# Performance work log

Measured on AMD Instinct MI355X. Metric: run time of the kernel, lower is better.

Reference implementation:

```python
import jax, jax.numpy as jnp
import numpy as np

D = 256; DFFN = 1024; H = 8; NLVL = 4; NPNT = 4; HD = D // H
BS = 4; NQ = 100; NPTS = 25
SPATIAL = [(128, 128), (64, 64), (32, 32), (16, 16)]
LEN_IN = sum(h * w for h, w in SPATIAL)


def _ln(x, g, b, eps=1e-5):
    m = x.mean(-1, keepdims=True)
    v = ((x - m) ** 2).mean(-1, keepdims=True)
    return (x - m) * jax.lax.rsqrt(v + eps) * g + b


def _mha(q, k, v, w_in, b_in, w_out, b_out):
    # torch nn.MultiheadAttention math, batch-first layout [B,S,D]
    B, Sq, _ = q.shape; Sk = k.shape[1]
    wq, wk, wv = jnp.split(w_in, 3, 0); bq, bk, bv = jnp.split(b_in, 3)
    qh = (q @ wq.T + bq).reshape(B, Sq, H, HD).transpose(0, 2, 1, 3)
    kh = (k @ wk.T + bk).reshape(B, Sk, H, HD).transpose(0, 2, 1, 3)
    vh = (v @ wv.T + bv).reshape(B, Sk, H, HD).transpose(0, 2, 1, 3)
    a = jax.nn.softmax(jnp.einsum('bhqd,bhkd->bhqk', qh, kh) * (1.0 / float(np.sqrt(HD))), -1)
    o = jnp.einsum('bhqk,bhkd->bhqd', a, vh).transpose(0, 2, 1, 3).reshape(B, Sq, D)
    return o @ w_out.T + b_out


def _msdeform(query, ref, src, off_w, off_b, aw_w, aw_b, val_w, val_b, out_w, out_b):
    # MSDeformAttn: per-query multi-level bilinear sampling + weighted aggregation
    bs, Lq, _ = query.shape
    value = (src @ val_w.T + val_b).reshape(bs, LEN_IN, H, HD)
    off = (query @ off_w.T + off_b).reshape(bs, Lq, H, NLVL, NPNT, 2)
    aw = jax.nn.softmax((query @ aw_w.T + aw_b).reshape(bs, Lq, H, NLVL * NPNT), -1)
    aw = aw.reshape(bs, Lq, H, NLVL, NPNT)
    norm = jnp.array([[w, h] for h, w in SPATIAL], jnp.float32)  # (W,H) per level
    loc = ref[:, :, None, :, None, :] + off / norm[None, None, None, :, None, :]
    out = jnp.zeros((bs, H, Lq, HD), query.dtype)
    start = 0
    for l, (hh, ww) in enumerate(SPATIAL):
        v_l = value[:, start:start + hh * ww].transpose(0, 2, 1, 3)  # [bs,H,hw,HD]
        start += hh * ww
        # grid_sample align_corners=False pixel coords: loc*size - 0.5
        x = (loc[:, :, :, l, :, 0] * ww - 0.5).transpose(0, 2, 1, 3).reshape(bs, H, Lq * NPNT)
        y = (loc[:, :, :, l, :, 1] * hh - 0.5).transpose(0, 2, 1, 3).reshape(bs, H, Lq * NPNT)
        x0 = jnp.floor(x); y0 = jnp.floor(y); wx = x - x0; wy = y - y0
        x0i = x0.astype(jnp.int32); y0i = y0.astype(jnp.int32); x1i = x0i + 1; y1i = y0i + 1
        def g(xi, yi):
            valid = ((xi >= 0) & (xi < ww) & (yi >= 0) & (yi < hh)).astype(query.dtype)
            idx = jnp.clip(yi, 0, hh - 1) * ww + jnp.clip(xi, 0, ww - 1)
            return jnp.take_along_axis(v_l, idx[..., None], axis=2) * valid[..., None]
        s = (g(x0i, y0i) * ((1 - wx) * (1 - wy))[..., None]
             + g(x1i, y0i) * (wx * (1 - wy))[..., None]
             + g(x0i, y1i) * ((1 - wx) * wy)[..., None]
             + g(x1i, y1i) * (wx * wy)[..., None])
        s = s.reshape(bs, H, Lq, NPNT, HD)
        out = out + (s * aw[:, :, :, l].transpose(0, 2, 1, 3)[..., None]).sum(3)
    return out.transpose(0, 2, 1, 3).reshape(bs, Lq, D) @ out_w.T + out_b


def _fwd(tgt, query_pos, reference_points, src,
         w_in_intra, b_in_intra, w_out_intra, b_out_intra, g_norm_intra, b_norm_intra,
         w_in_inter, b_in_inter, w_out_inter, b_out_inter, g_norm_inter, b_norm_inter,
         off_w, off_b, aw_w, aw_b, val_w, val_b, co_w, co_b, g_norm_cross, b_norm_cross,
         lin1_w, lin1_b, lin2_w, lin2_b, g_norm3, b_norm3):
    bs, nq, npts, d = tgt.shape
    # intra-instance self-attention (over control points)
    q = (tgt + query_pos).reshape(bs * nq, npts, d)
    t2 = _mha(q, q, tgt.reshape(bs * nq, npts, d), w_in_intra, b_in_intra, w_out_intra, b_out_intra)
    tgt = _ln(tgt + t2.reshape(bs, nq, npts, d), g_norm_intra, b_norm_intra)
    # inter-instance self-attention (over queries), no pos embed per source code
    ti = tgt.transpose(0, 2, 1, 3).reshape(bs * npts, nq, d)
    t2 = _mha(ti, ti, ti, w_in_inter, b_in_inter, w_out_inter, b_out_inter)
    ti = _ln(ti + t2, g_norm_inter, b_norm_inter).reshape(bs, npts, nq, d).transpose(0, 2, 1, 3)
    # deformable cross-attention
    ref = jnp.broadcast_to(reference_points[:, :, None], (bs, nq, npts, NLVL, 2)).reshape(bs, nq * npts, NLVL, 2)
    qc = (ti + query_pos).reshape(bs, nq * npts, d)
    t2 = _msdeform(qc, ref, src, off_w, off_b, aw_w, aw_b, val_w, val_b, co_w, co_b).reshape(bs, nq, npts, d)
    tgt = _ln(ti + t2, g_norm_cross, b_norm_cross)
    # FFN
    ff = jax.nn.relu(tgt @ lin1_w.T + lin1_b) @ lin2_w.T + lin2_b
    return _ln(tgt + ff, g_norm3, b_norm3)


def setup_inputs() -> dict:
    key = jax.random.key(0)
    ki = iter(jax.random.split(key, 40))
    def rn(shape, sc=0.02):
        return jax.random.normal(next(ki), shape, jnp.float32) * sc
    inp = dict(
        tgt=jax.random.normal(next(ki), (BS, NQ, NPTS, D), jnp.float32),
        query_pos=jax.random.normal(next(ki), (BS, NQ, NPTS, D), jnp.float32),
        reference_points=jax.random.uniform(next(ki), (BS, NQ, NLVL, 2), jnp.float32),
        src=jax.random.normal(next(ki), (BS, LEN_IN, D), jnp.float32),
        w_in_intra=rn((3 * D, D)), b_in_intra=jnp.zeros((3 * D,), jnp.float32),
        w_out_intra=rn((D, D)), b_out_intra=jnp.zeros((D,), jnp.float32),
        g_norm_intra=jnp.ones((D,), jnp.float32), b_norm_intra=jnp.zeros((D,), jnp.float32),
        w_in_inter=rn((3 * D, D)), b_in_inter=jnp.zeros((3 * D,), jnp.float32),
        w_out_inter=rn((D, D)), b_out_inter=jnp.zeros((D,), jnp.float32),
        g_norm_inter=jnp.ones((D,), jnp.float32), b_norm_inter=jnp.zeros((D,), jnp.float32),
        off_w=rn((H * NLVL * NPNT * 2, D), 0.001), off_b=rn((H * NLVL * NPNT * 2,), 0.5),
        aw_w=rn((H * NLVL * NPNT, D)), aw_b=jnp.zeros((H * NLVL * NPNT,), jnp.float32),
        val_w=rn((D, D)), val_b=jnp.zeros((D,), jnp.float32),
        co_w=rn((D, D)), co_b=jnp.zeros((D,), jnp.float32),
        g_norm_cross=jnp.ones((D,), jnp.float32), b_norm_cross=jnp.zeros((D,), jnp.float32),
        lin1_w=rn((DFFN, D)), lin1_b=jnp.zeros((DFFN,), jnp.float32),
        lin2_w=rn((D, DFFN)), lin2_b=jnp.zeros((D,), jnp.float32),
        g_norm3=jnp.ones((D,), jnp.float32), b_norm3=jnp.zeros((D,), jnp.float32),
        src_spatial_shapes=jnp.array(SPATIAL, jnp.int32),
        level_start_index=jnp.array(np.cumsum([0] + [h * w for h, w in SPATIAL[:-1]]), jnp.int32),
    )
    return inp


def reference(tgt, query_pos, reference_points, src,
              w_in_intra, b_in_intra, w_out_intra, b_out_intra, g_norm_intra, b_norm_intra,
              w_in_inter, b_in_inter, w_out_inter, b_out_inter, g_norm_inter, b_norm_inter,
              off_w, off_b, aw_w, aw_b, val_w, val_b, co_w, co_b, g_norm_cross, b_norm_cross,
              lin1_w, lin1_b, lin2_w, lin2_b, g_norm3, b_norm3,
              src_spatial_shapes, level_start_index):
    # spatial shapes / level starts are compile-time constants (SPATIAL); args kept for signature parity
    return _fwd(tgt, query_pos, reference_points, src,
                w_in_intra, b_in_intra, w_out_intra, b_out_intra, g_norm_intra, b_norm_intra,
                w_in_inter, b_in_inter, w_out_inter, b_out_inter, g_norm_inter, b_norm_inter,
                off_w, off_b, aw_w, aw_b, val_w, val_b, co_w, co_b, g_norm_cross, b_norm_cross,
                lin1_w, lin1_b, lin2_w, lin2_b, g_norm3, b_norm3)
```

## Files before the change

### kernel.cpp

```cpp
#include <hip/hip_runtime.h>
#include <math.h>

#define DMODEL 256
#define HEADS  8
#define HDIM   32
#define BS     4
#define NQ     100
#define NPTS   25
#define LQ     2500
#define M10K   10000
#define LEN_IN 21760
#define MVAL   87040

typedef float f32x4 __attribute__((ext_vector_type(4)));
typedef short s16x8 __attribute__((ext_vector_type(8)));
typedef unsigned short u16;

static __device__ __forceinline__ short f2bf(float f) {
    unsigned u = __builtin_bit_cast(unsigned, f);
    u = (u + 0x7fffu + ((u >> 16) & 1u)) >> 16;
    return (short)u;
}
static __device__ __forceinline__ unsigned pack2(float lo, float hi) {
    return (unsigned)(u16)f2bf(lo) | ((unsigned)(u16)f2bf(hi) << 16);
}
static __device__ __forceinline__ float bf_lo(unsigned u) {
    return __builtin_bit_cast(float, u << 16);
}
static __device__ __forceinline__ float bf_hi(unsigned u) {
    return __builtin_bit_cast(float, u & 0xffff0000u);
}

__global__ __launch_bounds__(256) void convert_weights_kernel(
    const float* __restrict__ s0, const float* __restrict__ s1,
    const float* __restrict__ s2, const float* __restrict__ s3,
    const float* __restrict__ s4, const float* __restrict__ s5,
    const float* __restrict__ s6, const float* __restrict__ s7,
    const float* __restrict__ s8, const float* __restrict__ s9,
    u16* __restrict__ dst)
{
    int t8 = (blockIdx.x * 256 + threadIdx.x) * 8;
    if (t8 >= 1277952) return;
    const float* s; int base;
    if      (t8 <  196608) { s = s0; base = 0;       }
    else if (t8 <  262144) { s = s1; base = 196608;  }
    else if (t8 <  458752) { s = s2; base = 262144;  }
    else if (t8 <  524288) { s = s3; base = 458752;  }
    else if (t8 <  589824) { s = s4; base = 524288;  }
    else if (t8 <  622592) { s = s5; base = 589824;  }
    else if (t8 <  688128) { s = s6; base = 622592;  }
    else if (t8 <  753664) { s = s7; base = 688128;  }
    else if (t8 < 1015808) { s = s8; base = 753664;  }
    else                   { s = s9; base = 1015808; }
    const float* p = s + (t8 - base);
    float4 a = *(const float4*)p;
    float4 b = *(const float4*)(p + 4);
    s16x8 v;
    v[0]=f2bf(a.x); v[1]=f2bf(a.y); v[2]=f2bf(a.z); v[3]=f2bf(a.w);
    v[4]=f2bf(b.x); v[5]=f2bf(b.y); v[6]=f2bf(b.z); v[7]=f2bf(b.w);
    *(s16x8*)(dst + t8) = v;
}

__global__ __launch_bounds__(256) void add_convert_kernel(
    const float* __restrict__ a, const float* __restrict__ b,
    u16* __restrict__ xb, u16* __restrict__ ab, int n8)
{
    int i = blockIdx.x * 256 + threadIdx.x;
    if (i >= n8) return;
    size_t o = (size_t)i * 8;
    float4 a0 = *(const float4*)(a + o);
    float4 a1 = *(const float4*)(a + o + 4);
    if (ab) {
        s16x8 v;
        v[0]=f2bf(a0.x); v[1]=f2bf(a0.y); v[2]=f2bf(a0.z); v[3]=f2bf(a0.w);
        v[4]=f2bf(a1.x); v[5]=f2bf(a1.y); v[6]=f2bf(a1.z); v[7]=f2bf(a1.w);
        *(s16x8*)(ab + o) = v;
    }
    if (b) {
        float4 b0 = *(const float4*)(b + o);
        float4 b1 = *(const float4*)(b + o + 4);
        a0.x += b0.x; a0.y += b0.y; a0.z += b0.z; a0.w += b0.w;
        a1.x += b1.x; a1.y += b1.y; a1.z += b1.z; a1.w += b1.w;
    }
    s16x8 v;
    v[0]=f2bf(a0.x); v[1]=f2bf(a0.y); v[2]=f2bf(a0.z); v[3]=f2bf(a0.w);
    v[4]=f2bf(a1.x); v[5]=f2bf(a1.y); v[6]=f2bf(a1.z); v[7]=f2bf(a1.w);
    *(s16x8*)(xb + o) = v;
}

#define LDSK 40

__global__ __launch_bounds__(256) void gemm_mfma_kernel(
    const void* __restrict__ Av, int a_bf16, int lda,
    const u16* __restrict__ W, int K,
    const float* __restrict__ bias,
    void* __restrict__ Cv, int ldc,
    int M, int relu, int out_bf16)
{
    __shared__ short As[64 * LDSK];
    __shared__ short Ws[64 * LDSK];

    const int tid = threadIdx.x;
    const int m0 = blockIdx.y * 64, n0 = blockIdx.x * 64;

    const int srow = tid >> 2;
    const int skseg = (tid & 3) * 8;

    const int wave = tid >> 6;
    const int wm = wave & 1, wn = wave >> 1;
    const int lane = tid & 63;
    const int lrow = lane & 15;
    const int kq = lane >> 4;

    f32x4 acc[2][2];
#pragma unroll
    for (int i = 0; i < 2; ++i)
#pragma unroll
        for (int j = 0; j < 2; ++j) acc[i][j] = (f32x4)(0.f);

    for (int k0 = 0; k0 < K; k0 += 32) {
        int gm = m0 + srow;
        s16x8 av = (s16x8)0;
        if (a_bf16) {
            if (gm < M)
                av = *(const s16x8*)((const u16*)Av + (size_t)gm * lda + k0 + skseg);
        } else {
            if (gm < M) {
                const float* ap = (const float*)Av + (size_t)gm * lda + k0 + skseg;
                float4 a0 = *(const float4*)ap;
                float4 a1 = *(const float4*)(ap + 4);
                av[0]=f2bf(a0.x); av[1]=f2bf(a0.y); av[2]=f2bf(a0.z); av[3]=f2bf(a0.w);
                av[4]=f2bf(a1.x); av[5]=f2bf(a1.y); av[6]=f2bf(a1.z); av[7]=f2bf(a1.w);
            }
        }
        s16x8 wv = *(const s16x8*)(W + (size_t)(n0 + srow) * K + k0 + skseg);
        *(s16x8*)&As[srow * LDSK + skseg] = av;
        *(s16x8*)&Ws[srow * LDSK + skseg] = wv;
        __syncthreads();

        s16x8 af[2], bf[2];
#pragma unroll
        for (int i = 0; i < 2; ++i)
            af[i] = *(const s16x8*)&As[(wm * 32 + i * 16 + lrow) * LDSK + kq * 8];
#pragma unroll
        for (int j = 0; j < 2; ++j)
            bf[j] = *(const s16x8*)&Ws[(wn * 32 + j * 16 + lrow) * LDSK + kq * 8];
#pragma unroll
        for (int i = 0; i < 2; ++i)
#pragma unroll
            for (int j = 0; j < 2; ++j)
                acc[i][j] = __builtin_amdgcn_mfma_f32_16x16x32_bf16(af[i], bf[j], acc[i][j], 0, 0, 0);
        __syncthreads();
    }

#pragma unroll
    for (int i = 0; i < 2; ++i) {
#pragma unroll
        for (int j = 0; j < 2; ++j) {
            int col = n0 + wn * 32 + j * 16 + lrow;
            float bv = bias[col];
#pragma unroll
            for (int reg = 0; reg < 4; ++reg) {
                int gm = m0 + wm * 32 + i * 16 + kq * 4 + reg;
                if (gm < M) {
                    float v = acc[i][j][reg] + bv;
                    if (relu) v = fmaxf(v, 0.f);
                    if (out_bf16)
                        ((u16*)Cv)[(size_t)gm * ldc + col] = (u16)f2bf(v);
                    else
                        ((float*)Cv)[(size_t)gm * ldc + col] = v;
                }
            }
        }
    }
}

__global__ void small_attn_kernel(const float* __restrict__ qkv,
                                  u16* __restrict__ out,
                                  int S, float scale)
{
    extern __shared__ float lds[];
    const int b = blockIdx.x, h = blockIdx.y;
    const float* base = qkv + (size_t)b * S * 768;

    for (int idx = threadIdx.x; idx < S * 64; idx += blockDim.x) {
        int r = idx >> 6, c = idx & 63;
        float v = (c < 32) ? base[r * 768 + 256 + h * 32 + c]
                           : base[r * 768 + 512 + h * 32 + (c - 32)];
        lds[idx] = v;
    }
    __syncthreads();

    const int i = threadIdx.x;
    if (i < S) {
        float q[32];
        const float* qp = base + i * 768 + h * 32;
#pragma unroll
        for (int c = 0; c < 32; ++c) q[c] = qp[c];
        float m = -1e30f, l = 0.f, acc[32];
#pragma unroll
        for (int c = 0; c < 32; ++c) acc[c] = 0.f;
        for (int j = 0; j < S; ++j) {
            const float* kj = &lds[j * 64];
            float s = 0.f;
#pragma unroll
            for (int c = 0; c < 32; ++c) s = fmaf(q[c], kj[c], s);
            s *= scale;
            float mn = fmaxf(m, s);
            float alpha = __expf(m - mn);
            float p = __expf(s - mn);
            l = l * alpha + p;
            const float* vj = kj + 32;
#pragma unroll
            for (int c = 0; c < 32; ++c) acc[c] = acc[c] * alpha + p * vj[c];
            m = mn;
        }
        float inv = 1.f / l;
        unsigned* op = (unsigned*)(out + ((size_t)b * S + i) * 256 + h * 32);
#pragma unroll
        for (int c = 0; c < 16; ++c)
            op[c] = pack2(acc[2 * c] * inv, acc[2 * c + 1] * inv);
    }
}

__global__ __launch_bounds__(64) void add_ln_kernel(
    const float* __restrict__ a, const float* __restrict__ b,
    const float* __restrict__ g, const float* __restrict__ beta,
    float* __restrict__ out, u16* __restrict__ out_bf, int transpose_mode)
{
    const int r = blockIdx.x;
    const int lane = threadIdx.x;
    const float* ar = a + (size_t)r * 256;
    const float* br = b + (size_t)r * 256;
    float x[4];
    float s = 0.f;
#pragma unroll
    for (int i = 0; i < 4; ++i) {
        x[i] = ar[lane + 64 * i] + br[lane + 64 * i];
        s += x[i];
    }
#pragma unroll
    for (int off = 32; off >= 1; off >>= 1) s += __shfl_xor(s, off);
    float mean = s * (1.f / 256.f);
    float vs = 0.f;
#pragma unroll
    for (int i = 0; i < 4; ++i) { float d = x[i] - mean; vs += d * d; }
#pragma unroll
    for (int off = 32; off >= 1; off >>= 1) vs += __shfl_xor(vs, off);
    float rstd = rsqrtf(vs * (1.f / 256.f) + 1e-5f);

    size_t ro = r;
    if (transpose_mode) {
        int q = r % 100; int bp = r / 100; int p = bp % 25; int bb = bp / 25;
        ro = ((size_t)bb * 100 + q) * 25 + p;
    }
    float* orow = out + ro * 256;
    u16* brow = out_bf ? out_bf + ro * 256 : (u16*)0;
#pragma unroll
    for (int i = 0; i < 4; ++i) {
        int c = lane + 64 * i;
        float v = (x[i] - mean) * rstd * g[c] + beta[c];
        orow[c] = v;
        if (brow) brow[c] = (u16)f2bf(v);
    }
}

__global__ __launch_bounds__(64) void tgt_to_ti_kernel(
    const float* __restrict__ tgt1, float* __restrict__ ti, u16* __restrict__ tib)
{
    const int r = blockIdx.x;
    int q = r % 100; int bp = r / 100; int p = bp % 25; int b = bp / 25;
    const float4* srcp = (const float4*)(tgt1 + (((size_t)b * 100 + q) * 25 + p) * 256);
    float4 v = srcp[threadIdx.x];
    ((float4*)(ti + (size_t)r * 256))[threadIdx.x] = v;
    uint2 pk = make_uint2(pack2(v.x, v.y), pack2(v.z, v.w));
    ((uint2*)(tib + (size_t)r * 256))[threadIdx.x] = pk;
}

__global__ __launch_bounds__(256, 4) void msdeform_sample_kernel(
    const u16* __restrict__ value,
    const float* __restrict__ off,
    const float* __restrict__ awl,
    const float* __restrict__ refp,
    u16* __restrict__ sampled)
{
    const int unit = blockIdx.x * 8 + (threadIdx.x >> 5);
    const int t = threadIdx.x & 31;
    const int h = t >> 2, c8 = t & 3;
    const int b = unit / LQ, lq = unit - b * LQ;
    const int q = lq / NPTS;

    const float* awp = awl + (size_t)unit * 128 + h * 16;
    float w[16];
    float mx = -1e30f;
#pragma unroll
    for (int k = 0; k < 16; ++k) { w[k] = awp[k]; mx = fmaxf(mx, w[k]); }
    float sum = 0.f;
#pragma unroll
    for (int k = 0; k < 16; ++k) { w[k] = __expf(w[k] - mx); sum += w[k]; }
    const float inv = 1.f / sum;

    const float* offp = off + (size_t)unit * 256 + h * 32;
    const float* rp = refp + ((size_t)b * 100 + q) * 8;
    const u16* vbase = value + (size_t)b * LEN_IN * 256 + h * 32 + c8 * 8;

    float acc[8];
#pragma unroll
    for (int k = 0; k < 8; ++k) acc[k] = 0.f;

    int start = 0;
    const int sz[4] = {128, 64, 32, 16};
#pragma unroll
    for (int l = 0; l < 4; ++l) {
        const int hh = sz[l], ww = sz[l];
        const float rx = rp[l * 2 + 0], ry = rp[l * 2 + 1];
#pragma unroll 1
        for (int pt = 0; pt < 4; ++pt) {
            float ox = offp[(l * 4 + pt) * 2 + 0];
            float oy = offp[(l * 4 + pt) * 2 + 1];
            float x = rx * ww + ox - 0.5f;
            float y = ry * hh + oy - 0.5f;
            float x0f = floorf(x), y0f = floorf(y);
            float wx = x - x0f, wy = y - y0f;
            int x0 = (int)x0f, y0 = (int)y0f;
            int x1 = x0 + 1, y1 = y0 + 1;
            float aw = w[l * 4 + pt] * inv;

            int x0c = min(max(x0, 0), ww - 1), x1c = min(max(x1, 0), ww - 1);
            int y0c = min(max(y0, 0), hh - 1), y1c = min(max(y1, 0), hh - 1);
            float w00 = aw * (1.f - wx) * (1.f - wy);
            float w10 = aw * wx * (1.f - wy);
            float w01 = aw * (1.f - wx) * wy;
            float w11 = aw * wx * wy;
            if (!(x0 >= 0 && x0 < ww)) { w00 = 0.f; w01 = 0.f; }
            if (!(x1 >= 0 && x1 < ww)) { w10 = 0.f; w11 = 0.f; }
            if (!(y0 >= 0 && y0 < hh)) { w00 = 0.f; w10 = 0.f; }
            if (!(y1 >= 0 && y1 < hh)) { w01 = 0.f; w11 = 0.f; }

            uint4 u00 = *(const uint4*)(vbase + (size_t)(start + y0c * ww + x0c) * 256);
            uint4 u10 = *(const uint4*)(vbase + (size_t)(start + y0c * ww + x1c) * 256);
            uint4 u01 = *(const uint4*)(vbase + (size_t)(start + y1c * ww + x0c) * 256);
            uint4 u11 = *(const uint4*)(vbase + (size_t)(start + y1c * ww + x1c) * 256);

#define ACC4(u, wgt) \
            acc[0] = fmaf(wgt, bf_lo(u.x), acc[0]); \
            acc[1] = fmaf(wgt, bf_hi(u.x), acc[1]); \
            acc[2] = fmaf(wgt, bf_lo(u.y), acc[2]); \
            acc[3] = fmaf(wgt, bf_hi(u.y), acc[3]); \
            acc[4] = fmaf(wgt, bf_lo(u.z), acc[4]); \
            acc[5] = fmaf(wgt, bf_hi(u.z), acc[5]); \
            acc[6] = fmaf(wgt, bf_lo(u.w), acc[6]); \
            acc[7] = fmaf(wgt, bf_hi(u.w), acc[7]);
            ACC4(u00, w00); ACC4(u10, w10); ACC4(u01, w01); ACC4(u11, w11);
#undef ACC4
        }
        start += hh * ww;
    }

    uint4 pk;
    pk.x = pack2(acc[0], acc[1]); pk.y = pack2(acc[2], acc[3]);
    pk.z = pack2(acc[4], acc[5]); pk.w = pack2(acc[6], acc[7]);
    *(uint4*)(sampled + (size_t)unit * 256 + h * 32 + c8 * 8) = pk;
}

extern "C" void kernel_launch(void* const* d_in, const int* in_sizes, int n_in,
                              void* d_out, int out_size, void* d_ws, size_t ws_size,
                              hipStream_t stream)
{
    (void)in_sizes; (void)n_in; (void)out_size; (void)ws_size;

    const float* tgt        = (const float*)d_in[0];
    const float* query_pos  = (const float*)d_in[1];
    const float* refp       = (const float*)d_in[2];
    const float* src        = (const float*)d_in[3];
    const float* w_in_intra = (const float*)d_in[4];
    const float* b_in_intra = (const float*)d_in[5];
    const float* w_out_intra= (const float*)d_in[6];
    const float* b_out_intra= (const float*)d_in[7];
    const float* g_ln_intra = (const float*)d_in[8];
    const float* b_ln_intra = (const float*)d_in[9];
    const float* w_in_inter = (const float*)d_in[10];
    const float* b_in_inter = (const float*)d_in[11];
    const float* w_out_inter= (const float*)d_in[12];
    const float* b_out_inter= (const float*)d_in[13];
    const float* g_ln_inter = (const float*)d_in[14];
    const float* b_ln_inter = (const float*)d_in[15];
    const float* off_w      = (const float*)d_in[16];
    const float* off_b      = (const float*)d_in[17];
    const float* aw_w       = (const float*)d_in[18];
    const float* aw_b       = (const float*)d_in[19];
    const float* val_w      = (const float*)d_in[20];
    const float* val_b      = (const float*)d_in[21];
    const float* co_w       = (const float*)d_in[22];
    const float* co_b       = (const float*)d_in[23];
    const float* g_ln_cross = (const float*)d_in[24];
    const float* b_ln_cross = (const float*)d_in[25];
    const float* lin1_w     = (const float*)d_in[26];
    const float* lin1_b     = (const float*)d_in[27];
    const float* lin2_w     = (const float*)d_in[28];
    const float* lin2_b     = (const float*)d_in[29];
    const float* g_ln3      = (const float*)d_in[30];
    const float* b_ln3      = (const float*)d_in[31];

    float* ws    = (float*)d_ws;
    float* qkv   = ws;
    float* tmp   = ws + 7680000;
    u16*   attnb = (u16*)(ws + 10240000);
    float* tgt1  = ws + 11520000;
    float* ti    = ws + 14080000;
    u16*   tib   = (u16*)(ws + 16640000);
    float* tA    = ws + 17920000;
    u16*   qcb   = (u16*)(ws + 20480000);
    u16*   x1b   = (u16*)(ws + 21760000);
    u16*   tgtb  = (u16*)(ws + 23040000);
    float* awl   = ws + 24320000;
    u16*   valueb= (u16*)(ws + 25600000);
    u16*   wb    = (u16*)(ws + 36741120);
    float* out   = (float*)d_out;

    u16* wb_in_intra  = wb;
    u16* wb_out_intra = wb + 196608;
    u16* wb_in_inter  = wb + 262144;
    u16* wb_out_inter = wb + 458752;
    u16* wb_off       = wb + 524288;
    u16* wb_aw        = wb + 589824;
    u16* wb_val       = wb + 622592;
    u16* wb_co        = wb + 688128;
    u16* wb_lin1      = wb + 753664;
    u16* wb_lin2      = wb + 1015808;

    const float scale = 0.17677669529663687f;
    const int MB10K = (M10K + 63) / 64;

    convert_weights_kernel<<<624, 256, 0, stream>>>(
        w_in_intra, w_out_intra, w_in_inter, w_out_inter, off_w,
        aw_w, val_w, co_w, lin1_w, lin2_w, wb);
    add_convert_kernel<<<1250, 256, 0, stream>>>(tgt, query_pos, x1b, tgtb, 320000);

    gemm_mfma_kernel<<<dim3(8, MB10K), 256, 0, stream>>>(x1b, 1, 256, wb_in_intra, 256,
                                                         b_in_intra, qkv, 768, M10K, 0, 0);
    gemm_mfma_kernel<<<dim3(4, MB10K), 256, 0, stream>>>(tgtb, 1, 256, wb_in_intra + 512 * 256, 256,
                                                         b_in_intra + 512, qkv + 512, 768, M10K, 0, 0);
    small_attn_kernel<<<dim3(400, 8), 64, 25 * 64 * 4, stream>>>(qkv, attnb, 25, scale);
    gemm_mfma_kernel<<<dim3(4, MB10K), 256, 0, stream>>>(attnb, 1, 256, wb_out_intra, 256,
                                                         b_out_intra, tmp, 256, M10K, 0, 0);
    add_ln_kernel<<<M10K, 64, 0, stream>>>(tgt, tmp, g_ln_intra, b_ln_intra, tgt1, (u16*)0, 0);

    tgt_to_ti_kernel<<<M10K, 64, 0, stream>>>(tgt1, ti, tib);
    gemm_mfma_kernel<<<dim3(12, MB10K), 256, 0, stream>>>(tib, 1, 256, wb_in_inter, 256,
                                                          b_in_inter, qkv, 768, M10K, 0, 0);
    small_attn_kernel<<<dim3(100, 8), 128, 100 * 64 * 4, stream>>>(qkv, attnb, 100, scale);
    gemm_mfma_kernel<<<dim3(4, MB10K), 256, 0, stream>>>(attnb, 1, 256, wb_out_inter, 256,
                                                         b_out_inter, tmp, 256, M10K, 0, 0);
    add_ln_kernel<<<M10K, 64, 0, stream>>>(ti, tmp, g_ln_inter, b_ln_inter, tA, (u16*)0, 1);

    add_convert_kernel<<<1250, 256, 0, stream>>>(tA, query_pos, qcb, (u16*)0, 320000);
    gemm_mfma_kernel<<<dim3(4, 1360), 256, 0, stream>>>(src, 0, 256, wb_val, 256,
                                                        val_b, valueb, 256, MVAL, 0, 1);
    gemm_mfma_kernel<<<dim3(4, MB10K), 256, 0, stream>>>(qcb, 1, 256, wb_off, 256,
                                                         off_b, tgt1, 256, M10K, 0, 0);
    gemm_mfma_kernel<<<dim3(2, MB10K), 256, 0, stream>>>(qcb, 1, 256, wb_aw, 256,
                                                         aw_b, awl, 128, M10K, 0, 0);
    msdeform_sample_kernel<<<1250, 256, 0, stream>>>(valueb, tgt1, awl, refp, attnb);
    gemm_mfma_kernel<<<dim3(4, MB10K), 256, 0, stream>>>(attnb, 1, 256, wb_co, 256,
                                                         co_b, tmp, 256, M10K, 0, 0);
    add_ln_kernel<<<M10K, 64, 0, stream>>>(tA, tmp, g_ln_cross, b_ln_cross, ti, tib, 0);

    gemm_mfma_kernel<<<dim3(16, MB10K), 256, 0, stream>>>(tib, 1, 256, wb_lin1, 256,
                                                          lin1_b, valueb, 1024, M10K, 1, 1);
    gemm_mfma_kernel<<<dim3(4, MB10K), 256, 0, stream>>>(valueb, 1, 1024, wb_lin2, 1024,
                                                         lin2_b, tmp, 256, M10K, 0, 0);
    add_ln_kernel<<<M10K, 64, 0, stream>>>(ti, tmp, g_ln3, b_ln3, out, (u16*)0, 0);
}
```

Baseline: 562.4 us.

## Specialize intra/inter attention kernels with key-split softmax and vectorized LDS loads

Replaces the generic small attention kernel with two specialized kernels. The intra kernel processes all 8 heads of one batch group per 256-thread block and loads K/V with float4. The inter kernel splits the 100 keys across 4 thread groups (512 threads), each running an online softmax, then merges the partial max/sum/accumulators through shared memory with serialized additions. This aims to raise parallelism and occupancy for the inter attention, which previously ran only 100 active threads per block over 100 keys, at the cost of extra barriers and a merge step.

```diff
diff --git a/kernel.cpp b/kernel.cpp
--- a/kernel.cpp
+++ b/kernel.cpp
@@ -175,51 +175,166 @@
     }
 }
 
-__global__ void small_attn_kernel(const float* __restrict__ qkv,
-                                  u16* __restrict__ out,
-                                  int S, float scale)
-{
-    extern __shared__ float lds[];
+__global__ __launch_bounds__(512) void inter_attn_kernel(
+    const float* __restrict__ qkv, u16* __restrict__ out, float scale)
+{
+    __shared__ float4 Kv[100][16];
+    __shared__ float4 Ml4[100];
+    __shared__ float4 Ll4[100];
+    __shared__ float  O[100][33];
+
     const int b = blockIdx.x, h = blockIdx.y;
-    const float* base = qkv + (size_t)b * S * 768;
-
-    for (int idx = threadIdx.x; idx < S * 64; idx += blockDim.x) {
-        int r = idx >> 6, c = idx & 63;
-        float v = (c < 32) ? base[r * 768 + 256 + h * 32 + c]
-                           : base[r * 768 + 512 + h * 32 + (c - 32)];
-        lds[idx] = v;
+    const float* base = qkv + (size_t)b * 100 * 768;
+    const int tid = threadIdx.x;
+    const int r = tid & 127, kc = tid >> 7;
+
+    for (int idx = tid; idx < 1600; idx += 512) {
+        int row = idx >> 4, seg = idx & 15;
+        const float* src = (seg < 8)
+            ? base + row * 768 + 256 + h * 32 + seg * 4
+            : base + row * 768 + 512 + h * 32 + (seg - 8) * 4;
+        Kv[row][seg] = *(const float4*)src;
+    }
+    for (int idx = tid; idx < 100 * 33; idx += 512)
+        ((float*)O)[idx] = 0.f;
+
+    float q[32];
+    if (r < 100) {
+        const float* qp = base + r * 768 + h * 32;
+#pragma unroll
+        for (int c4 = 0; c4 < 8; ++c4) {
+            float4 f = *(const float4*)(qp + c4 * 4);
+            q[c4*4+0] = f.x; q[c4*4+1] = f.y; q[c4*4+2] = f.z; q[c4*4+3] = f.w;
+        }
     }
     __syncthreads();
 
-    const int i = threadIdx.x;
-    if (i < S) {
-        float q[32];
-        const float* qp = base + i * 768 + h * 32;
-#pragma unroll
-        for (int c = 0; c < 32; ++c) q[c] = qp[c];
+    float m = -1e30f, l = 0.f, acc[32];
+#pragma unroll
+    for (int c = 0; c < 32; ++c) acc[c] = 0.f;
+
+    if (r < 100) {
+        const int j0 = kc * 25;
+#pragma unroll 2
+        for (int s = 0; s < 25; ++s) {
+            const float4* kr = &Kv[j0 + s][0];
+            float dot = 0.f;
+#pragma unroll
+            for (int c4 = 0; c4 < 8; ++c4) {
+                float4 kf = kr[c4];
+                dot = fmaf(q[c4*4+0], kf.x, dot);
+                dot = fmaf(q[c4*4+1], kf.y, dot);
+                dot = fmaf(q[c4*4+2], kf.z, dot);
+                dot = fmaf(q[c4*4+3], kf.w, dot);
+            }
+            dot *= scale;
+            float mn = fmaxf(m, dot);
+            float alpha = __expf(m - mn);
+            float p = __expf(dot - mn);
+            l = l * alpha + p;
+            const float4* vr = &Kv[j0 + s][8];
+#pragma unroll
+            for (int c4 = 0; c4 < 8; ++c4) {
+                float4 vf = vr[c4];
+                acc[c4*4+0] = acc[c4*4+0] * alpha + p * vf.x;
+                acc[c4*4+1] = acc[c4*4+1] * alpha + p * vf.y;
+                acc[c4*4+2] = acc[c4*4+2] * alpha + p * vf.z;
+                acc[c4*4+3] = acc[c4*4+3] * alpha + p * vf.w;
+            }
+            m = mn;
+        }
+        ((float*)&Ml4[r])[kc] = m;
+        ((float*)&Ll4[r])[kc] = l;
+    }
+    __syncthreads();
+
+    float alphaK = 0.f, Ltot = 1.f;
+    if (r < 100) {
+        float4 mv = Ml4[r];
+        float4 lv = Ll4[r];
+        float M = fmaxf(fmaxf(mv.x, mv.y), fmaxf(mv.z, mv.w));
+        Ltot = __expf(mv.x - M) * lv.x + __expf(mv.y - M) * lv.y
+             + __expf(mv.z - M) * lv.z + __expf(mv.w - M) * lv.w;
+        alphaK = __expf(m - M);
+    }
+    for (int cc = 0; cc < 4; ++cc) {
+        if (kc == cc && r < 100) {
+#pragma unroll
+            for (int c = 0; c < 32; ++c) O[r][c] += alphaK * acc[c];
+        }
+        __syncthreads();
+    }
+    if (kc == 0 && r < 100) {
+        float inv = 1.f / Ltot;
+        unsigned* op = (unsigned*)(out + ((size_t)b * 100 + r) * 256 + h * 32);
+#pragma unroll
+        for (int c = 0; c < 16; ++c)
+            op[c] = pack2(O[r][2*c] * inv, O[r][2*c+1] * inv);
+    }
+}
+
+__global__ __launch_bounds__(256) void intra_attn_kernel(
+    const float* __restrict__ qkv, u16* __restrict__ out, float scale)
+{
+    __shared__ float4 KV[25][128];
+
+    const int b = blockIdx.x;
+    const int h = threadIdx.x >> 5, r = threadIdx.x & 31;
+    const float* base = qkv + (size_t)b * 25 * 768;
+
+    for (int idx = threadIdx.x; idx < 3200; idx += 256) {
+        int row = idx >> 7, c = idx & 127;
+        KV[row][c] = *(const float4*)(base + row * 768 + 256 + c * 4);
+    }
+
+    float q[32];
+    if (r < 25) {
+        const float* qp = base + r * 768 + h * 32;
+#pragma unroll
+        for (int c4 = 0; c4 < 8; ++c4) {
+            float4 f = *(const float4*)(qp + c4 * 4);
+            q[c4*4+0] = f.x; q[c4*4+1] = f.y; q[c4*4+2] = f.z; q[c4*4+3] = f.w;
+        }
+    }
+    __syncthreads();
+
+    if (r < 25) {
         float m = -1e30f, l = 0.f, acc[32];
 #pragma unroll
         for (int c = 0; c < 32; ++c) acc[c] = 0.f;
-        for (int j = 0; j < S; ++j) {
-            const float* kj = &lds[j * 64];
-            float s = 0.f;
-#pragma unroll
-            for (int c = 0; c < 32; ++c) s = fmaf(q[c], kj[c], s);
-            s *= scale;
-            float mn = fmaxf(m, s);
+#pragma unroll 2
+        for (int j = 0; j < 25; ++j) {
+            const float4* kr = &KV[j][h * 8];
+            float dot = 0.f;
+#pragma unroll
+            for (int c4 = 0; c4 < 8; ++c4) {
+                float4 kf = kr[c4];
+                dot = fmaf(q[c4*4+0], kf.x, dot);
+                dot = fmaf(q[c4*4+1], kf.y, dot);
+                dot = fmaf(q[c4*4+2], kf.z, dot);
+                dot = fmaf(q[c4*4+3], kf.w, dot);
+            }
+            dot *= scale;
+            float mn = fmaxf(m, dot);
             float alpha = __expf(m - mn);
-            float p = __expf(s - mn);
+            float p = __expf(dot - mn);
             l = l * alpha + p;
-            const float* vj = kj + 32;
-#pragma unroll
-            for (int c = 0; c < 32; ++c) acc[c] = acc[c] * alpha + p * vj[c];
+            const float4* vr = &KV[j][64 + h * 8];
+#pragma unroll
+            for (int c4 = 0; c4 < 8; ++c4) {
+                float4 vf = vr[c4];
+                acc[c4*4+0] = acc[c4*4+0] * alpha + p * vf.x;
+                acc[c4*4+1] = acc[c4*4+1] * alpha + p * vf.y;
+                acc[c4*4+2] = acc[c4*4+2] * alpha + p * vf.z;
+                acc[c4*4+3] = acc[c4*4+3] * alpha + p * vf.w;
+            }
             m = mn;
         }
         float inv = 1.f / l;
-        unsigned* op = (unsigned*)(out + ((size_t)b * S + i) * 256 + h * 32);
+        unsigned* op = (unsigned*)(out + ((size_t)b * 25 + r) * 256 + h * 32);
 #pragma unroll
         for (int c = 0; c < 16; ++c)
-            op[c] = pack2(acc[2 * c] * inv, acc[2 * c + 1] * inv);
+            op[c] = pack2(acc[2*c] * inv, acc[2*c+1] * inv);
     }
 }
 
@@ -441,7 +556,7 @@
                                                          b_in_intra, qkv, 768, M10K, 0, 0);
     gemm_mfma_kernel<<<dim3(4, MB10K), 256, 0, stream>>>(tgtb, 1, 256, wb_in_intra + 512 * 256, 256,
                                                          b_in_intra + 512, qkv + 512, 768, M10K, 0, 0);
-    small_attn_kernel<<<dim3(400, 8), 64, 25 * 64 * 4, stream>>>(qkv, attnb, 25, scale);
+    intra_attn_kernel<<<400, 256, 0, stream>>>(qkv, attnb, scale);
     gemm_mfma_kernel<<<dim3(4, MB10K), 256, 0, stream>>>(attnb, 1, 256, wb_out_intra, 256,
                                                          b_out_intra, tmp, 256, M10K, 0, 0);
     add_ln_kernel<<<M10K, 64, 0, stream>>>(tgt, tmp, g_ln_intra, b_ln_intra, tgt1, (u16*)0, 0);
@@ -449,7 +564,7 @@
     tgt_to_ti_kernel<<<M10K, 64, 0, stream>>>(tgt1, ti, tib);
     gemm_mfma_kernel<<<dim3(12, MB10K), 256, 0, stream>>>(tib, 1, 256, wb_in_inter, 256,
                                                           b_in_inter, qkv, 768, M10K, 0, 0);
-    small_attn_kernel<<<dim3(100, 8), 128, 100 * 64 * 4, stream>>>(qkv, attnb, 100, scale);
+    inter_attn_kernel<<<dim3(100, 8), 512, 0, stream>>>(qkv, attnb, scale);
     gemm_mfma_kernel<<<dim3(4, MB10K), 256, 0, stream>>>(attnb, 1, 256, wb_out_inter, 256,
                                                          b_out_inter, tmp, 256, M10K, 0, 0);
     add_ln_kernel<<<M10K, 64, 0, stream>>>(ti, tmp, g_ln_inter, b_ln_inter, tA, (u16*)0, 1);
```

Result: faster. 524.2 us (-6.8%).
